# Kernel optimization log

Hardware: AMD Instinct MI355X
Metric: run time of the kernel (lower is better)

Reference implementation:

```python
import jax, jax.numpy as jnp
import numpy as np
import math

N_EMBD = 1024
BLOCK_SIZE = 2048
B = 4

def setup_inputs() -> dict:
    key = jax.random.key(0)
    ks = jax.random.split(key, 9)
    s = 0.02
    return {
        "q": jax.random.normal(ks[0], (B, BLOCK_SIZE, N_EMBD), jnp.float32),
        "k": jax.random.normal(ks[1], (B, BLOCK_SIZE, N_EMBD), jnp.float32),
        "v": jax.random.normal(ks[2], (B, BLOCK_SIZE, N_EMBD), jnp.float32),
        "wq_w": jax.random.normal(ks[3], (N_EMBD, N_EMBD), jnp.float32) * s,
        "wq_b": jax.random.normal(ks[4], (N_EMBD,), jnp.float32) * s,
        "wk_w": jax.random.normal(ks[5], (N_EMBD, N_EMBD), jnp.float32) * s,
        "wk_b": jax.random.normal(ks[6], (N_EMBD,), jnp.float32) * s,
        "wv_w": jax.random.normal(ks[7], (N_EMBD, N_EMBD), jnp.float32) * s,
        "wv_b": jax.random.normal(ks[8], (N_EMBD,), jnp.float32) * s,
        "causal": 1,
    }

def reference(q, k, v, wq_w, wq_b, wk_w, wk_b, wv_w, wv_b, causal):
    # torch Linear: y = x @ W.T + b
    qp = jnp.einsum('bte,oe->bto', q, wq_w) + wq_b
    kp = jnp.einsum('bte,oe->bto', k, wk_w) + wk_b
    vp = jnp.einsum('bte,oe->bto', v, wv_w) + wv_b
    scale = 1.0 / math.sqrt(N_EMBD)
    weights = jnp.einsum('bqe,bke->bqk', qp, kp) * scale  # [B,T1,T2]
    if causal:
        T1, T2 = qp.shape[1], kp.shape[1]
        mask = jnp.tril(jnp.ones((T1, T2), dtype=bool))
        weights = jnp.where(mask, weights, -jnp.inf)
    attn = jax.nn.softmax(weights, axis=-1)
    return jnp.einsum('bqk,bke->bqe', attn, vp)
```

## Files before the change

kernel.cpp:

```cpp
#include <hip/hip_runtime.h>
#include <hip/hip_bf16.h>
#include <cstdint>
#include <math.h>

#define T 2048
#define NE 1024
#define NB 4

typedef __attribute__((ext_vector_type(8))) short short8;
typedef __attribute__((ext_vector_type(4))) float floatx4;

__device__ __forceinline__ unsigned short f2bf(float f) {
    unsigned u = __float_as_uint(f);
    u += 0x7FFF + ((u >> 16) & 1);
    return (unsigned short)(u >> 16);
}

__device__ __forceinline__ short8 cvt8(floatx4 f0, floatx4 f1) {
    __hip_bfloat162 a = __float22bfloat162_rn(float2{f0[0], f0[1]});
    __hip_bfloat162 b = __float22bfloat162_rn(float2{f0[2], f0[3]});
    __hip_bfloat162 c = __float22bfloat162_rn(float2{f1[0], f1[1]});
    __hip_bfloat162 d = __float22bfloat162_rn(float2{f1[2], f1[3]});
    union { short8 s; unsigned u[4]; } r;
    r.u[0] = *(unsigned*)&a; r.u[1] = *(unsigned*)&b;
    r.u[2] = *(unsigned*)&c; r.u[3] = *(unsigned*)&d;
    return r.s;
}

__device__ __forceinline__ void gl2lds(const void* g, void* l) {
    __builtin_amdgcn_global_load_lds(
        (const __attribute__((address_space(1))) void*)g,
        (__attribute__((address_space(3))) void*)l, 16, 0, 0);
}

template<int BIAS_MODE, bool OUT_F32, bool TRIDEC, bool CKLIM, bool DUAL, int SWIZTN>
__global__ __launch_bounds__(256) void gemm_bf16(
    const unsigned short* __restrict__ A0, const unsigned short* __restrict__ A1,
    const unsigned short* __restrict__ B0, const unsigned short* __restrict__ B1,
    const float* __restrict__ bias0, const float* __restrict__ bias1,
    void* __restrict__ C0, void* __restrict__ C1,
    int K, int lda, int ldb, int ldc,
    size_t sA, size_t sB, size_t sC, float scale)
{
    int tm, tn;
    const int bz = blockIdx.z;
    if (TRIDEC) {
        int i = blockIdx.x;
        tm = (int)((sqrtf(8.f * (float)i + 1.f) - 1.f) * 0.5f);
        while ((tm + 1) * (tm + 2) / 2 <= i) ++tm;
        while (tm * (tm + 1) / 2 > i) --tm;
        tn = i - tm * (tm + 1) / 2;
    } else if (SWIZTN > 0) {
        const int bid = blockIdx.x, nper = gridDim.x >> 3;
        const int lin = (bid & 7) * nper + (bid >> 3);
        tm = lin / SWIZTN; tn = lin % SWIZTN;
    } else {
        tn = blockIdx.x;
        tm = CKLIM ? (int)(gridDim.y - 1 - blockIdx.y) : (int)blockIdx.y;
    }

    __shared__ __align__(16) char As[8192];
    __shared__ __align__(16) char Bs[8192];

    const int tid = threadIdx.x, lane = tid & 63, wave = tid >> 6;
    const int wm = wave & 1, wn = wave >> 1;
    const int quad = lane >> 4, l15 = lane & 15;

    const char* Ab = (const char*)((DUAL && bz) ? A1 : A0) + (size_t)bz * sA * 2;
    const char* Bb = (const char*)((DUAL && bz) ? B1 : B0) + (size_t)bz * sB * 2;
    const float* bias = (DUAL && bz) ? bias1 : bias0;

    int Keff = K;
    if (CKLIM) { int kl = (tm + 1) * 128; Keff = kl < K ? kl : K; }

    const size_t ldab = (size_t)lda * 2, ldbb = (size_t)ldb * 2;
    const char* gA = Ab + (size_t)(tm * 128 + wave * 16 + (lane >> 2)) * ldab + (size_t)(lane & 3) * 16;
    const char* gB = Bb + (size_t)(tn * 128 + wave * 16 + (lane >> 2)) * ldbb + (size_t)(lane & 3) * 16;
    char* lA = As + wave * 1024;
    char* lB = Bs + wave * 1024;

    floatx4 acc[4][4] = {};

    for (int k0 = 0; k0 < Keff; k0 += 32) {
        gl2lds(gA + (size_t)k0 * 2, lA);
        gl2lds(gA + 64 * ldab + (size_t)k0 * 2, lA + 4096);
        gl2lds(gB + (size_t)k0 * 2, lB);
        gl2lds(gB + 64 * ldbb + (size_t)k0 * 2, lB + 4096);
        __syncthreads();

        short8 af[4], bfr[4];
        #pragma unroll
        for (int i = 0; i < 4; i++)
            af[i] = *(const short8*)(As + (wm * 64 + i * 16 + l15) * 64 + quad * 16);
        #pragma unroll
        for (int j = 0; j < 4; j++)
            bfr[j] = *(const short8*)(Bs + (wn * 64 + j * 16 + l15) * 64 + quad * 16);

        #pragma unroll
        for (int i = 0; i < 4; i++)
            #pragma unroll
            for (int j = 0; j < 4; j++)
                acc[i][j] = __builtin_amdgcn_mfma_f32_16x16x32_bf16(af[i], bfr[j], acc[i][j], 0, 0, 0);
        __syncthreads();
    }

    char* Cb = (char*)((DUAL && bz) ? C1 : C0) + (size_t)bz * sC * (OUT_F32 ? 4 : 2);
    #pragma unroll
    for (int i = 0; i < 4; i++) {
        #pragma unroll
        for (int j = 0; j < 4; j++) {
            const int n = tn * 128 + wn * 64 + j * 16 + l15;
            #pragma unroll
            for (int r = 0; r < 4; r++) {
                const int m = tm * 128 + wm * 64 + i * 16 + quad * 4 + r;
                float val = acc[i][j][r] * scale;
                if (BIAS_MODE == 1) val += bias[n];
                if (BIAS_MODE == 2) val += bias[m];
                if (OUT_F32) ((float*)Cb)[(size_t)m * ldc + n] = val;
                else         ((unsigned short*)Cb)[(size_t)m * ldc + n] = f2bf(val);
            }
        }
    }
}

__global__ __launch_bounds__(256) void cvt_all(
    const float* __restrict__ q, const float* __restrict__ k, const float* __restrict__ v,
    const float* __restrict__ wq, const float* __restrict__ wk, const float* __restrict__ wv,
    unsigned short* __restrict__ qb, unsigned short* __restrict__ kb, unsigned short* __restrict__ vb,
    unsigned short* __restrict__ wqb, unsigned short* __restrict__ wkb, unsigned short* __restrict__ wvb)
{
    const int IN8 = NB * T * NE / 8;
    const int W8  = NE * NE / 8;
    int i = blockIdx.x * 256 + threadIdx.x;
    const float* s; unsigned short* d; int j;
    if (i < 3 * IN8) {
        int sel = i / IN8; j = i - sel * IN8;
        s = sel == 0 ? q : sel == 1 ? k : v;
        d = sel == 0 ? qb : sel == 1 ? kb : vb;
    } else {
        int t2 = i - 3 * IN8; int sel = t2 / W8; j = t2 - sel * W8;
        s = sel == 0 ? wq : sel == 1 ? wk : wv;
        d = sel == 0 ? wqb : sel == 1 ? wkb : wvb;
    }
    const floatx4* p = (const floatx4*)s;
    ((short8*)d)[j] = cvt8(p[2 * j], p[2 * j + 1]);
}

__global__ __launch_bounds__(256) void softmax_causal(unsigned short* __restrict__ S)
{
    const int row = blockIdx.x;
    const int b = row >> 11, r = row & 2047;
    unsigned short* p = S + ((size_t)b * T + (size_t)r) * T;
    const int nv = r + 1;
    const int tid = threadIdx.x, lane = tid & 63, wave = tid >> 6;
    const int c0 = tid * 8;

    short8 raw = ((const short8*)p)[tid];
    float x[8];
    float mx = -3.0e38f;
    #pragma unroll
    for (int j = 0; j < 8; j++) {
        float vv = -3.0e38f;
        if (c0 + j < nv) vv = __uint_as_float((unsigned)(unsigned short)raw[j] << 16);
        x[j] = vv;
        mx = fmaxf(mx, vv);
    }
    #pragma unroll
    for (int off = 32; off > 0; off >>= 1)
        mx = fmaxf(mx, __shfl_xor(mx, off));
    __shared__ float smax[4], ssum[4];
    if (lane == 0) smax[wave] = mx;
    __syncthreads();
    mx = fmaxf(fmaxf(smax[0], smax[1]), fmaxf(smax[2], smax[3]));

    float s = 0.f;
    #pragma unroll
    for (int j = 0; j < 8; j++) {
        float e = 0.f;
        if (c0 + j < nv) e = __expf(x[j] - mx);
        x[j] = e;
        s += e;
    }
    #pragma unroll
    for (int off = 32; off > 0; off >>= 1)
        s += __shfl_xor(s, off);
    if (lane == 0) ssum[wave] = s;
    __syncthreads();
    const float inv = 1.f / (ssum[0] + ssum[1] + ssum[2] + ssum[3]);

    short8 o;
    #pragma unroll
    for (int j = 0; j < 8; j++)
        o[j] = (short)f2bf(x[j] * inv);
    ((short8*)p)[tid] = o;
}

extern "C" void kernel_launch(void* const* d_in, const int* in_sizes, int n_in,
                              void* d_out, int out_size, void* d_ws, size_t ws_size,
                              hipStream_t stream)
{
    const float* q    = (const float*)d_in[0];
    const float* k    = (const float*)d_in[1];
    const float* v    = (const float*)d_in[2];
    const float* wq_w = (const float*)d_in[3];
    const float* wq_b = (const float*)d_in[4];
    const float* wk_w = (const float*)d_in[5];
    const float* wk_b = (const float*)d_in[6];
    const float* wv_w = (const float*)d_in[7];
    const float* wv_b = (const float*)d_in[8];

    const size_t INEL = (size_t)NB * T * NE;

    unsigned short* qp = (unsigned short*)d_out;
    unsigned short* kp = qp + INEL;

    unsigned short* vpT = (unsigned short*)d_ws;
    unsigned short* S   = vpT + (size_t)NB * NE * T;
    unsigned short* qb  = S;
    unsigned short* kb  = qb + INEL;
    unsigned short* vb  = kb + INEL;
    unsigned short* wqb = vb + INEL;
    unsigned short* wkb = wqb + (size_t)NE * NE;
    unsigned short* wvb = wkb + (size_t)NE * NE;

    dim3 blk(256);

    const int NCVT = (3 * (int)(INEL / 8) + 3 * NE * NE / 8 + 255) / 256;
    cvt_all<<<dim3(NCVT), blk, 0, stream>>>(q, k, v, wq_w, wk_w, wv_w, qb, kb, vb, wqb, wkb, wvb);

    gemm_bf16<1, false, false, false, true, 8><<<dim3(512, 1, 2), blk, 0, stream>>>(
        qb, kb, wqb, wkb, wq_b, wk_b, qp, kp, NE, NE, NE, NE, 0, 0, 0, 1.0f);

    gemm_bf16<2, false, false, false, false, 0><<<dim3(T/128, NE/128, NB), blk, 0, stream>>>(
        wvb, nullptr, vb, nullptr, wv_b, nullptr, vpT, nullptr,
        NE, NE, NE, T, 0, (size_t)T * NE, (size_t)NE * T, 1.0f);

    gemm_bf16<0, false, true, false, false, 0><<<dim3(136, 1, NB), blk, 0, stream>>>(
        qp, nullptr, kp, nullptr, nullptr, nullptr, S, nullptr,
        NE, NE, NE, T, (size_t)T * NE, (size_t)T * NE, (size_t)T * T, 0.03125f);

    softmax_causal<<<dim3(NB * T), blk, 0, stream>>>(S);

    gemm_bf16<0, true, false, true, false, 0><<<dim3(NE/128, T/128, NB), blk, 0, stream>>>(
        S, nullptr, vpT, nullptr, nullptr, nullptr, d_out, nullptr,
        T, T, T, NE, (size_t)T * T, (size_t)NE * T, (size_t)T * NE, 1.0f);
}
```

Before: 346.0 us.

## Double GEMM K-tile, add XCD-aware tile ordering, trim softmax to causal blocks

The GEMM main loop now stages a 64-wide K slice per iteration (32 KB LDS) instead of 32, which halves the number of barrier pairs per tile. The tile index mapping now interleaves blocks across the 8 XCDs: the QK^T triangular decode is remapped, and the PV GEMM pairs heavy and light causal rows per XCD to balance work. The softmax skips loading and storing columns beyond the 128-block causal limit, which the PV GEMM never reads. The larger LDS footprint may lower occupancy.

```diff
diff --git a/kernel.cpp b/kernel.cpp
--- a/kernel.cpp
+++ b/kernel.cpp
@@ -33,7 +33,7 @@
         (__attribute__((address_space(3))) void*)l, 16, 0, 0);
 }
 
-template<int BIAS_MODE, bool OUT_F32, bool TRIDEC, bool CKLIM, bool DUAL, int SWIZTN>
+template<int BIAS_MODE, bool OUT_F32, bool CKLIM, bool DUAL, int MODE>
 __global__ __launch_bounds__(256) void gemm_bf16(
     const unsigned short* __restrict__ A0, const unsigned short* __restrict__ A1,
     const unsigned short* __restrict__ B0, const unsigned short* __restrict__ B1,
@@ -44,23 +44,27 @@
 {
     int tm, tn;
     const int bz = blockIdx.z;
-    if (TRIDEC) {
-        int i = blockIdx.x;
-        tm = (int)((sqrtf(8.f * (float)i + 1.f) - 1.f) * 0.5f);
-        while ((tm + 1) * (tm + 2) / 2 <= i) ++tm;
-        while (tm * (tm + 1) / 2 > i) --tm;
-        tn = i - tm * (tm + 1) / 2;
-    } else if (SWIZTN > 0) {
-        const int bid = blockIdx.x, nper = gridDim.x >> 3;
-        const int lin = (bid & 7) * nper + (bid >> 3);
-        tm = lin / SWIZTN; tn = lin % SWIZTN;
+    if (MODE == 2) {
+        const int i = blockIdx.x;
+        int lin = (i & 7) * 17 + (i >> 3);
+        tm = (int)((sqrtf(8.f * (float)lin + 1.f) - 1.f) * 0.5f);
+        while ((tm + 1) * (tm + 2) / 2 <= lin) ++tm;
+        while (tm * (tm + 1) / 2 > lin) --tm;
+        tn = lin - tm * (tm + 1) / 2;
+    } else if (MODE == 1) {
+        const int bid = blockIdx.x;
+        const int lin = (bid & 7) * (gridDim.x >> 3) + (bid >> 3);
+        tm = lin >> 3; tn = lin & 7;
+    } else if (MODE == 3) {
+        const int xcd = blockIdx.x & 7, j = blockIdx.x >> 3;
+        tm = (j & 1) ? xcd : (15 - xcd);
+        tn = j >> 1;
     } else {
-        tn = blockIdx.x;
-        tm = CKLIM ? (int)(gridDim.y - 1 - blockIdx.y) : (int)blockIdx.y;
-    }
-
-    __shared__ __align__(16) char As[8192];
-    __shared__ __align__(16) char Bs[8192];
+        tn = blockIdx.x; tm = blockIdx.y;
+    }
+
+    __shared__ __align__(16) char As[16384];
+    __shared__ __align__(16) char Bs[16384];
 
     const int tid = threadIdx.x, lane = tid & 63, wave = tid >> 6;
     const int wm = wave & 1, wn = wave >> 1;
@@ -74,33 +78,38 @@
     if (CKLIM) { int kl = (tm + 1) * 128; Keff = kl < K ? kl : K; }
 
     const size_t ldab = (size_t)lda * 2, ldbb = (size_t)ldb * 2;
-    const char* gA = Ab + (size_t)(tm * 128 + wave * 16 + (lane >> 2)) * ldab + (size_t)(lane & 3) * 16;
-    const char* gB = Bb + (size_t)(tn * 128 + wave * 16 + (lane >> 2)) * ldbb + (size_t)(lane & 3) * 16;
+    const char* gA = Ab + (size_t)(tm * 128 + wave * 8 + (lane >> 3)) * ldab + (size_t)(lane & 7) * 16;
+    const char* gB = Bb + (size_t)(tn * 128 + wave * 8 + (lane >> 3)) * ldbb + (size_t)(lane & 7) * 16;
     char* lA = As + wave * 1024;
     char* lB = Bs + wave * 1024;
 
     floatx4 acc[4][4] = {};
 
-    for (int k0 = 0; k0 < Keff; k0 += 32) {
-        gl2lds(gA + (size_t)k0 * 2, lA);
-        gl2lds(gA + 64 * ldab + (size_t)k0 * 2, lA + 4096);
-        gl2lds(gB + (size_t)k0 * 2, lB);
-        gl2lds(gB + 64 * ldbb + (size_t)k0 * 2, lB + 4096);
+    for (int k0 = 0; k0 < Keff; k0 += 64) {
+        const size_t kb = (size_t)k0 * 2;
+        #pragma unroll
+        for (int c = 0; c < 4; ++c)
+            gl2lds(gA + (size_t)c * 32 * ldab + kb, lA + c * 4096);
+        #pragma unroll
+        for (int c = 0; c < 4; ++c)
+            gl2lds(gB + (size_t)c * 32 * ldbb + kb, lB + c * 4096);
         __syncthreads();
 
-        short8 af[4], bfr[4];
-        #pragma unroll
-        for (int i = 0; i < 4; i++)
-            af[i] = *(const short8*)(As + (wm * 64 + i * 16 + l15) * 64 + quad * 16);
-        #pragma unroll
-        for (int j = 0; j < 4; j++)
-            bfr[j] = *(const short8*)(Bs + (wn * 64 + j * 16 + l15) * 64 + quad * 16);
-
-        #pragma unroll
-        for (int i = 0; i < 4; i++)
+        #pragma unroll
+        for (int kk = 0; kk < 2; kk++) {
+            short8 af[4], bfr[4];
+            #pragma unroll
+            for (int i = 0; i < 4; i++)
+                af[i] = *(const short8*)(As + (wm * 64 + i * 16 + l15) * 128 + kk * 64 + quad * 16);
             #pragma unroll
             for (int j = 0; j < 4; j++)
-                acc[i][j] = __builtin_amdgcn_mfma_f32_16x16x32_bf16(af[i], bfr[j], acc[i][j], 0, 0, 0);
+                bfr[j] = *(const short8*)(Bs + (wn * 64 + j * 16 + l15) * 128 + kk * 64 + quad * 16);
+            #pragma unroll
+            for (int i = 0; i < 4; i++)
+                #pragma unroll
+                for (int j = 0; j < 4; j++)
+                    acc[i][j] = __builtin_amdgcn_mfma_f32_16x16x32_bf16(af[i], bfr[j], acc[i][j], 0, 0, 0);
+        }
         __syncthreads();
     }
 
@@ -152,10 +161,13 @@
     const int b = row >> 11, r = row & 2047;
     unsigned short* p = S + ((size_t)b * T + (size_t)r) * T;
     const int nv = r + 1;
+    const int lim = ((r >> 7) + 1) * 128;
     const int tid = threadIdx.x, lane = tid & 63, wave = tid >> 6;
     const int c0 = tid * 8;
-
-    short8 raw = ((const short8*)p)[tid];
+    const bool act = c0 < lim;
+
+    short8 raw = {};
+    if (act) raw = ((const short8*)p)[tid];
     float x[8];
     float mx = -3.0e38f;
     #pragma unroll
@@ -188,11 +200,13 @@
     __syncthreads();
     const float inv = 1.f / (ssum[0] + ssum[1] + ssum[2] + ssum[3]);
 
-    short8 o;
-    #pragma unroll
-    for (int j = 0; j < 8; j++)
-        o[j] = (short)f2bf(x[j] * inv);
-    ((short8*)p)[tid] = o;
+    if (act) {
+        short8 o;
+        #pragma unroll
+        for (int j = 0; j < 8; j++)
+            o[j] = (short)f2bf(x[j] * inv);
+        ((short8*)p)[tid] = o;
+    }
 }
 
 extern "C" void kernel_launch(void* const* d_in, const int* in_sizes, int n_in,
@@ -228,20 +242,20 @@
     const int NCVT = (3 * (int)(INEL / 8) + 3 * NE * NE / 8 + 255) / 256;
     cvt_all<<<dim3(NCVT), blk, 0, stream>>>(q, k, v, wq_w, wk_w, wv_w, qb, kb, vb, wqb, wkb, wvb);
 
-    gemm_bf16<1, false, false, false, true, 8><<<dim3(512, 1, 2), blk, 0, stream>>>(
+    gemm_bf16<1, false, false, true, 1><<<dim3(512, 1, 2), blk, 0, stream>>>(
         qb, kb, wqb, wkb, wq_b, wk_b, qp, kp, NE, NE, NE, NE, 0, 0, 0, 1.0f);
 
-    gemm_bf16<2, false, false, false, false, 0><<<dim3(T/128, NE/128, NB), blk, 0, stream>>>(
+    gemm_bf16<2, false, false, false, 0><<<dim3(T/128, NE/128, NB), blk, 0, stream>>>(
         wvb, nullptr, vb, nullptr, wv_b, nullptr, vpT, nullptr,
         NE, NE, NE, T, 0, (size_t)T * NE, (size_t)NE * T, 1.0f);
 
-    gemm_bf16<0, false, true, false, false, 0><<<dim3(136, 1, NB), blk, 0, stream>>>(
+    gemm_bf16<0, false, false, false, 2><<<dim3(136, 1, NB), blk, 0, stream>>>(
         qp, nullptr, kp, nullptr, nullptr, nullptr, S, nullptr,
         NE, NE, NE, T, (size_t)T * NE, (size_t)T * NE, (size_t)T * T, 0.03125f);
 
     softmax_causal<<<dim3(NB * T), blk, 0, stream>>>(S);
 
-    gemm_bf16<0, true, false, true, false, 0><<<dim3(NE/128, T/128, NB), blk, 0, stream>>>(
+    gemm_bf16<0, true, true, false, 3><<<dim3(128, 1, NB), blk, 0, stream>>>(
         S, nullptr, vpT, nullptr, nullptr, nullptr, d_out, nullptr,
         T, T, T, NE, (size_t)T * T, (size_t)NE * T, (size_t)T * NE, 1.0f);
 }
```

New measurement: 343.7 us. Within noise of the previous version (-0.7%).
